# Kernel optimization log

Hardware: AMD Instinct MI355X
Metric: run time of the kernel (lower is better)

## Reference

```python
import jax, jax.numpy as jnp
import numpy as np

DIM = 2048
RANK = 8
SCALE_INIT = 0.01
N_TOKENS = 8192


def setup_inputs() -> dict:
    key = jax.random.key(0)
    kx, ku, kv = jax.random.split(key, 3)
    x = jax.random.normal(kx, (N_TOKENS, DIM), dtype=jnp.float32)
    U = jax.random.normal(ku, (DIM, RANK), dtype=jnp.float32) * SCALE_INIT
    V = jax.random.normal(kv, (DIM, RANK), dtype=jnp.float32) * SCALE_INIT
    gate = jnp.float32(-2.0)
    return {"x": x, "U": U, "V": V, "gate": gate}


def reference(x, U, V, gate):
    # omega = (U V^T - V U^T) * sigmoid(gate)  -- skew-symmetric generator
    UV = U @ V.T                               # [dim, dim]
    omega = (UV - UV.T) * jax.nn.sigmoid(gate)
    I = jnp.eye(x.shape[-1], dtype=x.dtype)
    half = omega * 0.5
    # Cayley transform: R = (I - omega/2)^{-1} (I + omega/2)
    R = jnp.linalg.solve(I - half, I + half)   # [dim, dim]
    return x @ R.T
```

## Files before the change

### kernel.cpp

```cpp
#include <hip/hip_runtime.h>
#include <hip/hip_fp16.h>
#include <cstddef>

#define DIM 2048
#define NTOK 8192
#define NEUMANN_ITERS 6
#define PLANE (DIM / 2 + 1)


typedef _Float16 h4 __attribute__((ext_vector_type(4)));
typedef float f32x4 __attribute__((ext_vector_type(4)));

__device__ __forceinline__ unsigned pkh(float lo, float hi) {
  auto p = __builtin_amdgcn_cvt_pkrtz(lo, hi);
  return __builtin_bit_cast(unsigned, p);
}

__global__ __launch_bounds__(256) void rora_fused(
    const float* __restrict__ x, const float* __restrict__ U,
    const float* __restrict__ V, const float* __restrict__ gate,
    float* __restrict__ out) {
  __shared__ uint4 uvQ[4][PLANE];
  __shared__ float Gs[16][17];
  __shared__ float Ya[16][17];
  __shared__ float Yb[16][17];
  __shared__ float Wtw[16][17];
  __shared__ float As[16][17];
  __shared__ float Ared[4][64][4];
  __shared__ float Agred[4][64][4];
  const int t = threadIdx.x;
  const int lane = t & 63, wv = t >> 6;
  const int rA = lane & 15, g = lane >> 4;

  {
    const float4* U4 = (const float4*)U;
    const float4* V4 = (const float4*)V;
#pragma unroll
    for (int rep = 0; rep < 4; ++rep) {
      const int P = rep * 256 + t;
      const float4 a0 = U4[4 * P + 0], a1 = U4[4 * P + 1];
      const float4 a2 = U4[4 * P + 2], a3 = U4[4 * P + 3];
      const float4 b0 = V4[4 * P + 0], b1 = V4[4 * P + 1];
      const float4 b2 = V4[4 * P + 2], b3 = V4[4 * P + 3];
      uvQ[0][P] = make_uint4(pkh(a0.x, a2.x), pkh(a0.y, a2.y),
                             pkh(a0.z, a2.z), pkh(a0.w, a2.w));
      uvQ[1][P] = make_uint4(pkh(a1.x, a3.x), pkh(a1.y, a3.y),
                             pkh(a1.z, a3.z), pkh(a1.w, a3.w));
      uvQ[2][P] = make_uint4(pkh(b0.x, b2.x), pkh(b0.y, b2.y),
                             pkh(b0.z, b2.z), pkh(b0.w, b2.w));
      uvQ[3][P] = make_uint4(pkh(b1.x, b3.x), pkh(b1.y, b3.y),
                             pkh(b1.z, b3.z), pkh(b1.w, b3.w));
    }
  }
  __syncthreads();

  const int row0 = blockIdx.x * 16;
  {
    f32x4 acca = {0.f, 0.f, 0.f, 0.f};
    f32x4 accg = {0.f, 0.f, 0.f, 0.f};
    const float* xrow = x + (size_t)(row0 + rA) * DIM;
    const int q1 = rA >> 2, c1 = rA & 3;
    const unsigned* uvW = (const unsigned*)&uvQ[q1][0];
#pragma unroll 4
    for (int step = 0; step < 32; ++step) {
      const int d0 = wv * 512 + step * 16 + g * 4;
      const float4 xv = *(const float4*)(xrow + d0);
      uint2 au = {pkh(xv.x, xv.y), pkh(xv.z, xv.w)};
      const h4 af = __builtin_bit_cast(h4, au);
      const int P0 = d0 >> 1;
      uint2 bu = {uvW[P0 * 4 + c1], uvW[(P0 + 1) * 4 + c1]};
      const h4 bf = __builtin_bit_cast(h4, bu);
      acca = __builtin_amdgcn_mfma_f32_16x16x16f16(af, bf, acca, 0, 0, 0);
      accg = __builtin_amdgcn_mfma_f32_16x16x16f16(bf, bf, accg, 0, 0, 0);
    }
    Ared[wv][lane][0] = acca[0];
    Ared[wv][lane][1] = acca[1];
    Ared[wv][lane][2] = acca[2];
    Ared[wv][lane][3] = acca[3];
    Agred[wv][lane][0] = accg[0];
    Agred[wv][lane][1] = accg[1];
    Agred[wv][lane][2] = accg[2];
    Agred[wv][lane][3] = accg[3];
  }
  __syncthreads();
  {
    const int l = t & 63, j = t >> 6;
    const float sa = (Ared[0][l][j] + Ared[1][l][j]) +
                     (Ared[2][l][j] + Ared[3][l][j]);
    const float sgm = (Agred[0][l][j] + Agred[1][l][j]) +
                      (Agred[2][l][j] + Agred[3][l][j]);
    const int dr = (l >> 4) * 4 + j, dc = l & 15;
    As[dr][dc] = sa;
    Wtw[dr][dc] = sgm;
  }
  __syncthreads();

  const float sg = 1.f / (1.f + expf(-gate[0]));
  {
    const int r = t >> 4, c = t & 15;
    const float gv = (r < 8) ? sg * Wtw[r + 8][c] : -sg * Wtw[r - 8][c];
    Gs[r][c] = gv;
    Ya[r][c] = ((r == c) ? 1.f : 0.f) + 0.5f * gv;
  }
  __syncthreads();
#pragma unroll
  for (int m = 0; m < NEUMANN_ITERS; ++m) {
    const int r = t >> 4, c = t & 15;
    const float (*Yp)[17] = (m & 1) ? Yb : Ya;
    float (*Yn)[17] = (m & 1) ? Ya : Yb;
    float acc = ((r == c) ? 1.f : 0.f) + 0.5f * Gs[r][c];
#pragma unroll
    for (int j = 0; j < 16; ++j)
      acc = fmaf(0.5f * Gs[r][j], Yp[j][c], acc);
    Yn[r][c] = acc;
    __syncthreads();
  }

  h4 cf;
  {
    const float hs = 0.5f * sg;
    const int r = rA;
    float cj[4];
#pragma unroll
    for (int j = 0; j < 4; ++j) {
      const int k = g * 4 + j;
      float s = 0.f;
#pragma unroll
      for (int jj = 0; jj < 8; ++jj) {
        const float zA = Ya[k][jj] + ((k == jj) ? 1.f : 0.f);
        const float zB = Ya[k][8 + jj] + ((k == 8 + jj) ? 1.f : 0.f);
        s = fmaf(zA, As[r][8 + jj], s);
        s = fmaf(-zB, As[r][jj], s);
      }
      cj[j] = hs * s;
    }
    uint2 cu = {pkh(cj[0], cj[1]), pkh(cj[2], cj[3])};
    cf = __builtin_bit_cast(h4, cu);
  }

  {
    const int par = rA & 1;
    const float4* x4row = (const float4*)(x + (size_t)(row0 + rA) * DIM);
    float4* o4row = (float4*)(out + (size_t)(row0 + rA) * DIM);
    for (int nt = wv * 32; nt < wv * 32 + 32; ++nt) {
      const int dcol0 = nt * 16;
      const uint4 wq = uvQ[g][(dcol0 + rA) >> 1];
      const unsigned w01 = par ? ((wq.x >> 16) | (wq.y & 0xffff0000u))
                               : ((wq.x & 0xffffu) | (wq.y << 16));
      const unsigned w23 = par ? ((wq.z >> 16) | (wq.w & 0xffff0000u))
                               : ((wq.z & 0xffffu) | (wq.w << 16));
      uint2 bu = {w01, w23};
      const h4 bf = __builtin_bit_cast(h4, bu);
      f32x4 z4 = {0.f, 0.f, 0.f, 0.f};
      const f32x4 o = __builtin_amdgcn_mfma_f32_16x16x16f16(bf, cf, z4, 0, 0, 0);
      const int q4 = (dcol0 >> 2) + g;
      const float4 xv = x4row[q4];
      float4 ov;
      ov.x = xv.x + o[0];
      ov.y = xv.y + o[1];
      ov.z = xv.z + o[2];
      ov.w = xv.w + o[3];
      o4row[q4] = ov;
    }
  }
}

extern "C" void kernel_launch(void* const* d_in, const int* in_sizes, int n_in,
                              void* d_out, int out_size, void* d_ws, size_t ws_size,
                              hipStream_t stream) {
  const float* x    = (const float*)d_in[0];
  const float* U    = (const float*)d_in[1];
  const float* V    = (const float*)d_in[2];
  const float* gate = (const float*)d_in[3];
  float* out = (float*)d_out;

  rora_fused<<<NTOK / 16, 256, 0, stream>>>(x, U, V, gate, out);
}
```

Baseline: 40.58 us.

## Drop shared U/V staging; read U/V from global and halve rows per block

Removes the per-block staging of U and V into LDS as packed fp16 and its barrier. The MFMA operands are now built straight from strided global loads of U/V, which should mostly hit in cache. Each block now handles 8 token rows instead of 16, doubling the grid and leaving half of every 16-row MFMA tile idle (masked loads and stores). This raises parallelism and removes LDS pressure and prologue latency, but wastes MFMA lanes and issues many uncoalesced global reads of U/V.

New measurement: 51.72 us. 1.27x slower.

```diff
diff --git a/kernel.cpp b/kernel.cpp
--- a/kernel.cpp
+++ b/kernel.cpp
@@ -5,7 +5,6 @@
 #define DIM 2048
 #define NTOK 8192
 #define NEUMANN_ITERS 6
-#define PLANE (DIM / 2 + 1)
 
 
 typedef _Float16 h4 __attribute__((ext_vector_type(4)));
@@ -20,7 +19,6 @@
     const float* __restrict__ x, const float* __restrict__ U,
     const float* __restrict__ V, const float* __restrict__ gate,
     float* __restrict__ out) {
-  __shared__ uint4 uvQ[4][PLANE];
   __shared__ float Gs[16][17];
   __shared__ float Ya[16][17];
   __shared__ float Yb[16][17];
@@ -32,43 +30,24 @@
   const int lane = t & 63, wv = t >> 6;
   const int rA = lane & 15, g = lane >> 4;
 
-  {
-    const float4* U4 = (const float4*)U;
-    const float4* V4 = (const float4*)V;
-#pragma unroll
-    for (int rep = 0; rep < 4; ++rep) {
-      const int P = rep * 256 + t;
-      const float4 a0 = U4[4 * P + 0], a1 = U4[4 * P + 1];
-      const float4 a2 = U4[4 * P + 2], a3 = U4[4 * P + 3];
-      const float4 b0 = V4[4 * P + 0], b1 = V4[4 * P + 1];
-      const float4 b2 = V4[4 * P + 2], b3 = V4[4 * P + 3];
-      uvQ[0][P] = make_uint4(pkh(a0.x, a2.x), pkh(a0.y, a2.y),
-                             pkh(a0.z, a2.z), pkh(a0.w, a2.w));
-      uvQ[1][P] = make_uint4(pkh(a1.x, a3.x), pkh(a1.y, a3.y),
-                             pkh(a1.z, a3.z), pkh(a1.w, a3.w));
-      uvQ[2][P] = make_uint4(pkh(b0.x, b2.x), pkh(b0.y, b2.y),
-                             pkh(b0.z, b2.z), pkh(b0.w, b2.w));
-      uvQ[3][P] = make_uint4(pkh(b1.x, b3.x), pkh(b1.y, b3.y),
-                             pkh(b1.z, b3.z), pkh(b1.w, b3.w));
-    }
-  }
-  __syncthreads();
+  const float* Wcol = ((rA < 8) ? U : V) + (rA & 7);
 
-  const int row0 = blockIdx.x * 16;
+  const int row0 = blockIdx.x * 8;
   {
     f32x4 acca = {0.f, 0.f, 0.f, 0.f};
     f32x4 accg = {0.f, 0.f, 0.f, 0.f};
     const float* xrow = x + (size_t)(row0 + rA) * DIM;
-    const int q1 = rA >> 2, c1 = rA & 3;
-    const unsigned* uvW = (const unsigned*)&uvQ[q1][0];
+    const bool live = (rA < 8);
 #pragma unroll 4
     for (int step = 0; step < 32; ++step) {
       const int d0 = wv * 512 + step * 16 + g * 4;
-      const float4 xv = *(const float4*)(xrow + d0);
+      float4 xv = make_float4(0.f, 0.f, 0.f, 0.f);
+      if (live) xv = *(const float4*)(xrow + d0);
       uint2 au = {pkh(xv.x, xv.y), pkh(xv.z, xv.w)};
       const h4 af = __builtin_bit_cast(h4, au);
-      const int P0 = d0 >> 1;
-      uint2 bu = {uvW[P0 * 4 + c1], uvW[(P0 + 1) * 4 + c1]};
+      const float w0 = Wcol[8 * (d0 + 0)], w1 = Wcol[8 * (d0 + 1)];
+      const float w2 = Wcol[8 * (d0 + 2)], w3 = Wcol[8 * (d0 + 3)];
+      uint2 bu = {pkh(w0, w1), pkh(w2, w3)};
       const h4 bf = __builtin_bit_cast(h4, bu);
       acca = __builtin_amdgcn_mfma_f32_16x16x16f16(af, bf, acca, 0, 0, 0);
       accg = __builtin_amdgcn_mfma_f32_16x16x16f16(bf, bf, accg, 0, 0, 0);
@@ -139,28 +118,28 @@
   }
 
   {
-    const int par = rA & 1;
+    const float4* WB4 = (const float4*)((g < 2) ? U : V);
+    const int gsel = g & 1;
+    const bool live = (rA < 8);
     const float4* x4row = (const float4*)(x + (size_t)(row0 + rA) * DIM);
     float4* o4row = (float4*)(out + (size_t)(row0 + rA) * DIM);
     for (int nt = wv * 32; nt < wv * 32 + 32; ++nt) {
       const int dcol0 = nt * 16;
-      const uint4 wq = uvQ[g][(dcol0 + rA) >> 1];
-      const unsigned w01 = par ? ((wq.x >> 16) | (wq.y & 0xffff0000u))
-                               : ((wq.x & 0xffffu) | (wq.y << 16));
-      const unsigned w23 = par ? ((wq.z >> 16) | (wq.w & 0xffff0000u))
-                               : ((wq.z & 0xffffu) | (wq.w << 16));
-      uint2 bu = {w01, w23};
+      const float4 wf4 = WB4[(dcol0 + rA) * 2 + gsel];
+      uint2 bu = {pkh(wf4.x, wf4.y), pkh(wf4.z, wf4.w)};
       const h4 bf = __builtin_bit_cast(h4, bu);
       f32x4 z4 = {0.f, 0.f, 0.f, 0.f};
       const f32x4 o = __builtin_amdgcn_mfma_f32_16x16x16f16(bf, cf, z4, 0, 0, 0);
-      const int q4 = (dcol0 >> 2) + g;
-      const float4 xv = x4row[q4];
-      float4 ov;
-      ov.x = xv.x + o[0];
-      ov.y = xv.y + o[1];
-      ov.z = xv.z + o[2];
-      ov.w = xv.w + o[3];
-      o4row[q4] = ov;
+      if (live) {
+        const int q4 = (dcol0 >> 2) + g;
+        const float4 xv = x4row[q4];
+        float4 ov;
+        ov.x = xv.x + o[0];
+        ov.y = xv.y + o[1];
+        ov.z = xv.z + o[2];
+        ov.w = xv.w + o[3];
+        o4row[q4] = ov;
+      }
     }
   }
 }
@@ -174,5 +153,5 @@
   const float* gate = (const float*)d_in[3];
   float* out = (float*)d_out;
 
-  rora_fused<<<NTOK / 16, 256, 0, stream>>>(x, U, V, gate, out);
+  rora_fused<<<NTOK / 8, 256, 0, stream>>>(x, U, V, gate, out);
 }
```

## Process two 16-row tiles per 512-thread block, overlapping second projection with first output

Applied to the files above, without the earlier changes.

Each block now uses 512 threads and handles 32 rows as two 16-row tiles. The U/V fp16 staging into shared memory, the Gram matrix and the Neumann solve are paid once per block instead of once per 16 rows. The second tile's x·UV projection is interleaved with the first tile's output loop so its global loads overlap the first tile's stores. In exchange there are half as many blocks, more registers and extra barriers, and half the threads sit idle during the 16x16 Neumann iterations.

Result: slower. 41.64 us (+2.6%).

```diff
diff --git a/kernel.cpp b/kernel.cpp
--- a/kernel.cpp
+++ b/kernel.cpp
@@ -16,7 +16,7 @@
   return __builtin_bit_cast(unsigned, p);
 }
 
-__global__ __launch_bounds__(256) void rora_fused(
+__global__ __launch_bounds__(512) void rora_fused(
     const float* __restrict__ x, const float* __restrict__ U,
     const float* __restrict__ V, const float* __restrict__ gate,
     float* __restrict__ out) {
@@ -26,18 +26,19 @@
   __shared__ float Yb[16][17];
   __shared__ float Wtw[16][17];
   __shared__ float As[16][17];
-  __shared__ float Ared[4][64][4];
-  __shared__ float Agred[4][64][4];
+  __shared__ float Ared[8][64][4];
+  __shared__ float Agred[8][64][4];
   const int t = threadIdx.x;
   const int lane = t & 63, wv = t >> 6;
   const int rA = lane & 15, g = lane >> 4;
+  const int row0 = blockIdx.x * 32;
 
   {
     const float4* U4 = (const float4*)U;
     const float4* V4 = (const float4*)V;
 #pragma unroll
-    for (int rep = 0; rep < 4; ++rep) {
-      const int P = rep * 256 + t;
+    for (int rep = 0; rep < 2; ++rep) {
+      const int P = rep * 512 + t;
       const float4 a0 = U4[4 * P + 0], a1 = U4[4 * P + 1];
       const float4 a2 = U4[4 * P + 2], a3 = U4[4 * P + 3];
       const float4 b0 = V4[4 * P + 0], b1 = V4[4 * P + 1];
@@ -54,16 +55,16 @@
   }
   __syncthreads();
 
-  const int row0 = blockIdx.x * 16;
+  const int q1 = rA >> 2, c1 = rA & 3;
+  const unsigned* uvW = (const unsigned*)&uvQ[q1][0];
+
   {
     f32x4 acca = {0.f, 0.f, 0.f, 0.f};
     f32x4 accg = {0.f, 0.f, 0.f, 0.f};
     const float* xrow = x + (size_t)(row0 + rA) * DIM;
-    const int q1 = rA >> 2, c1 = rA & 3;
-    const unsigned* uvW = (const unsigned*)&uvQ[q1][0];
 #pragma unroll 4
-    for (int step = 0; step < 32; ++step) {
-      const int d0 = wv * 512 + step * 16 + g * 4;
+    for (int step = 0; step < 16; ++step) {
+      const int d0 = wv * 256 + step * 16 + g * 4;
       const float4 xv = *(const float4*)(xrow + d0);
       uint2 au = {pkh(xv.x, xv.y), pkh(xv.z, xv.w)};
       const h4 af = __builtin_bit_cast(h4, au);
@@ -73,22 +74,18 @@
       acca = __builtin_amdgcn_mfma_f32_16x16x16f16(af, bf, acca, 0, 0, 0);
       accg = __builtin_amdgcn_mfma_f32_16x16x16f16(bf, bf, accg, 0, 0, 0);
     }
-    Ared[wv][lane][0] = acca[0];
-    Ared[wv][lane][1] = acca[1];
-    Ared[wv][lane][2] = acca[2];
-    Ared[wv][lane][3] = acca[3];
-    Agred[wv][lane][0] = accg[0];
-    Agred[wv][lane][1] = accg[1];
-    Agred[wv][lane][2] = accg[2];
-    Agred[wv][lane][3] = accg[3];
-  }
-  __syncthreads();
-  {
+#pragma unroll
+    for (int j = 0; j < 4; ++j) {
+      Ared[wv][lane][j] = acca[j];
+      Agred[wv][lane][j] = accg[j];
+    }
+  }
+  __syncthreads();
+  if (t < 256) {
     const int l = t & 63, j = t >> 6;
-    const float sa = (Ared[0][l][j] + Ared[1][l][j]) +
-                     (Ared[2][l][j] + Ared[3][l][j]);
-    const float sgm = (Agred[0][l][j] + Agred[1][l][j]) +
-                      (Agred[2][l][j] + Agred[3][l][j]);
+    float sa = 0.f, sgm = 0.f;
+#pragma unroll
+    for (int w = 0; w < 8; ++w) { sa += Ared[w][l][j]; sgm += Agred[w][l][j]; }
     const int dr = (l >> 4) * 4 + j, dc = l & 15;
     As[dr][dc] = sa;
     Wtw[dr][dc] = sgm;
@@ -96,7 +93,7 @@
   __syncthreads();
 
   const float sg = 1.f / (1.f + expf(-gate[0]));
-  {
+  if (t < 256) {
     const int r = t >> 4, c = t & 15;
     const float gv = (r < 8) ? sg * Wtw[r + 8][c] : -sg * Wtw[r - 8][c];
     Gs[r][c] = gv;
@@ -105,21 +102,22 @@
   __syncthreads();
 #pragma unroll
   for (int m = 0; m < NEUMANN_ITERS; ++m) {
-    const int r = t >> 4, c = t & 15;
-    const float (*Yp)[17] = (m & 1) ? Yb : Ya;
-    float (*Yn)[17] = (m & 1) ? Ya : Yb;
-    float acc = ((r == c) ? 1.f : 0.f) + 0.5f * Gs[r][c];
-#pragma unroll
-    for (int j = 0; j < 16; ++j)
-      acc = fmaf(0.5f * Gs[r][j], Yp[j][c], acc);
-    Yn[r][c] = acc;
+    if (t < 256) {
+      const int r = t >> 4, c = t & 15;
+      const float (*Yp)[17] = (m & 1) ? Yb : Ya;
+      float (*Yn)[17] = (m & 1) ? Ya : Yb;
+      float acc = ((r == c) ? 1.f : 0.f) + 0.5f * Gs[r][c];
+#pragma unroll
+      for (int j = 0; j < 16; ++j)
+        acc = fmaf(0.5f * Gs[r][j], Yp[j][c], acc);
+      Yn[r][c] = acc;
+    }
     __syncthreads();
   }
 
-  h4 cf;
-  {
-    const float hs = 0.5f * sg;
-    const int r = rA;
+  const float hs = 0.5f * sg;
+  h4 cf0;
+  {
     float cj[4];
 #pragma unroll
     for (int j = 0; j < 4; ++j) {
@@ -129,21 +127,89 @@
       for (int jj = 0; jj < 8; ++jj) {
         const float zA = Ya[k][jj] + ((k == jj) ? 1.f : 0.f);
         const float zB = Ya[k][8 + jj] + ((k == 8 + jj) ? 1.f : 0.f);
-        s = fmaf(zA, As[r][8 + jj], s);
-        s = fmaf(-zB, As[r][jj], s);
+        s = fmaf(zA, As[rA][8 + jj], s);
+        s = fmaf(-zB, As[rA][jj], s);
       }
       cj[j] = hs * s;
     }
     uint2 cu = {pkh(cj[0], cj[1]), pkh(cj[2], cj[3])};
-    cf = __builtin_bit_cast(h4, cu);
-  }
-
-  {
+    cf0 = __builtin_bit_cast(h4, cu);
+  }
+
+  f32x4 acca1 = {0.f, 0.f, 0.f, 0.f};
+  {
+    const float* xrow1 = x + (size_t)(row0 + 16 + rA) * DIM;
+    const float4* x4row0 = (const float4*)(x + (size_t)(row0 + rA) * DIM);
+    float4* o4row0 = (float4*)(out + (size_t)(row0 + rA) * DIM);
     const int par = rA & 1;
-    const float4* x4row = (const float4*)(x + (size_t)(row0 + rA) * DIM);
-    float4* o4row = (float4*)(out + (size_t)(row0 + rA) * DIM);
-    for (int nt = wv * 32; nt < wv * 32 + 32; ++nt) {
-      const int dcol0 = nt * 16;
+#pragma unroll 2
+    for (int i = 0; i < 16; ++i) {
+      const int d0 = wv * 256 + i * 16 + g * 4;
+      const float4 xv = *(const float4*)(xrow1 + d0);
+      const int dcol0 = (wv * 16 + i) * 16;
+      const uint4 wq = uvQ[g][(dcol0 + rA) >> 1];
+      const unsigned w01 = par ? ((wq.x >> 16) | (wq.y & 0xffff0000u))
+                               : ((wq.x & 0xffffu) | (wq.y << 16));
+      const unsigned w23 = par ? ((wq.z >> 16) | (wq.w & 0xffff0000u))
+                               : ((wq.z & 0xffffu) | (wq.w << 16));
+      uint2 b2u = {w01, w23};
+      const h4 bf2 = __builtin_bit_cast(h4, b2u);
+      f32x4 z4 = {0.f, 0.f, 0.f, 0.f};
+      const f32x4 o = __builtin_amdgcn_mfma_f32_16x16x16f16(bf2, cf0, z4, 0, 0, 0);
+      const int q4 = (dcol0 >> 2) + g;
+      const float4 xv0 = x4row0[q4];
+      float4 ov;
+      ov.x = xv0.x + o[0];
+      ov.y = xv0.y + o[1];
+      ov.z = xv0.z + o[2];
+      ov.w = xv0.w + o[3];
+      o4row0[q4] = ov;
+      uint2 au = {pkh(xv.x, xv.y), pkh(xv.z, xv.w)};
+      const h4 af = __builtin_bit_cast(h4, au);
+      const int P0 = d0 >> 1;
+      uint2 bu = {uvW[P0 * 4 + c1], uvW[(P0 + 1) * 4 + c1]};
+      const h4 bf = __builtin_bit_cast(h4, bu);
+      acca1 = __builtin_amdgcn_mfma_f32_16x16x16f16(af, bf, acca1, 0, 0, 0);
+    }
+  }
+#pragma unroll
+  for (int j = 0; j < 4; ++j) Ared[wv][lane][j] = acca1[j];
+  __syncthreads();
+  if (t < 256) {
+    const int l = t & 63, j = t >> 6;
+    float sa = 0.f;
+#pragma unroll
+    for (int w = 0; w < 8; ++w) sa += Ared[w][l][j];
+    As[(l >> 4) * 4 + j][l & 15] = sa;
+  }
+  __syncthreads();
+
+  h4 cf1;
+  {
+    float cj[4];
+#pragma unroll
+    for (int j = 0; j < 4; ++j) {
+      const int k = g * 4 + j;
+      float s = 0.f;
+#pragma unroll
+      for (int jj = 0; jj < 8; ++jj) {
+        const float zA = Ya[k][jj] + ((k == jj) ? 1.f : 0.f);
+        const float zB = Ya[k][8 + jj] + ((k == 8 + jj) ? 1.f : 0.f);
+        s = fmaf(zA, As[rA][8 + jj], s);
+        s = fmaf(-zB, As[rA][jj], s);
+      }
+      cj[j] = hs * s;
+    }
+    uint2 cu = {pkh(cj[0], cj[1]), pkh(cj[2], cj[3])};
+    cf1 = __builtin_bit_cast(h4, cu);
+  }
+
+  {
+    const int par = rA & 1;
+    const float4* x4row1 = (const float4*)(x + (size_t)(row0 + 16 + rA) * DIM);
+    float4* o4row1 = (float4*)(out + (size_t)(row0 + 16 + rA) * DIM);
+    for (int i = 0; i < 16; ++i) {
+      const int dcol0 = (wv * 16 + i) * 16;
       const uint4 wq = uvQ[g][(dcol0 + rA) >> 1];
       const unsigned w01 = par ? ((wq.x >> 16) | (wq.y & 0xffff0000u))
                                : ((wq.x & 0xffffu) | (wq.y << 16));
@@ -152,15 +218,15 @@
       uint2 bu = {w01, w23};
       const h4 bf = __builtin_bit_cast(h4, bu);
       f32x4 z4 = {0.f, 0.f, 0.f, 0.f};
-      const f32x4 o = __builtin_amdgcn_mfma_f32_16x16x16f16(bf, cf, z4, 0, 0, 0);
+      const f32x4 o = __builtin_amdgcn_mfma_f32_16x16x16f16(bf, cf1, z4, 0, 0, 0);
       const int q4 = (dcol0 >> 2) + g;
-      const float4 xv = x4row[q4];
+      const float4 xv = x4row1[q4];
       float4 ov;
       ov.x = xv.x + o[0];
       ov.y = xv.y + o[1];
       ov.z = xv.z + o[2];
       ov.w = xv.w + o[3];
-      o4row[q4] = ov;
+      o4row1[q4] = ov;
     }
   }
 }
@@ -174,5 +240,5 @@
   const float* gate = (const float*)d_in[3];
   float* out = (float*)d_out;
 
-  rora_fused<<<NTOK / 16, 256, 0, stream>>>(x, U, V, gate, out);
+  rora_fused<<<NTOK / 32, 512, 0, stream>>>(x, U, V, gate, out);
 }
```
